# Performance work log

Measured on AMD Instinct MI355X. Metric: run time of the kernel, lower is better.

Reference implementation:

```python
import jax, jax.numpy as jnp
import numpy as np

N_NODES = 100000
N_EDGES = 1600000
IN_FEAT = 128
HID_FEAT = 128
OUT_FEAT = 128


def setup_inputs() -> dict:
    key = jax.random.key(0)
    k1, k2, k3, k4, k5 = jax.random.split(key, 5)
    x = jax.random.normal(k1, (N_NODES, IN_FEAT), dtype=jnp.float32)
    # Xavier-ish scale for weights
    W_in = jax.random.normal(k2, (2, IN_FEAT, HID_FEAT), dtype=jnp.float32) * (1.0 / np.sqrt(IN_FEAT))
    W_out = jax.random.normal(k3, (2, HID_FEAT, OUT_FEAT), dtype=jnp.float32) * (1.0 / np.sqrt(HID_FEAT))
    src = jax.random.randint(k4, (N_EDGES,), 0, N_NODES, dtype=jnp.int32)
    dst = jax.random.randint(k5, (N_EDGES,), 0, N_NODES, dtype=jnp.int32)
    return {"x": x, "W_in": W_in, "W_out": W_out, "src": src, "dst": dst}


def _mean_aggregate(h, src, dst, num_nodes):
    # copy_src('h','m') + fn.mean('m','neigh'): gather src feats, segment-mean by dst.
    msgs = h[src]                                             # [E, D]
    summed = jax.ops.segment_sum(msgs, dst, num_segments=num_nodes)   # [N, D]
    deg = jax.ops.segment_sum(jnp.ones((src.shape[0],), h.dtype), dst,
                              num_segments=num_nodes)         # [N]
    deg = jnp.maximum(deg, 1.0)                               # zero-in-degree -> 0 output
    return summed / deg[:, None]


def reference(x, W_in, W_out, src, dst):
    n = x.shape[0]
    # Layer 0 (i == 0): uses weight_in, ReLU activation (i != K-1)
    neigh = _mean_aggregate(x, src, dst, n)
    h = x @ W_in[0] + neigh @ W_in[1]
    h = jax.nn.relu(h)
    # Layer 1 (i == K-1): uses weight_out, no activation
    neigh = _mean_aggregate(h, src, dst, n)
    h = h @ W_out[0] + neigh @ W_out[1]
    return h
```

## Files before the change

### kernel.cpp

```cpp
#include <hip/hip_runtime.h>

#define NF 128
#define NBSHIFT 8
#define NBMAX 512
#define CHUNK 4096
#define DCHUNK 4096

typedef __attribute__((ext_vector_type(8))) short bf16x8;
typedef __attribute__((ext_vector_type(4))) float f32x4;
typedef __attribute__((ext_vector_type(2))) float f32x2;

__device__ __forceinline__ unsigned short f2bf(float f) {
    unsigned int u = __builtin_bit_cast(unsigned int, f);
    u = (u + 0x7fffu + ((u >> 16) & 1u)) >> 16;
    return (unsigned short)u;
}
__device__ __forceinline__ float bflo(unsigned int u) {
    return __builtin_bit_cast(float, u << 16);
}
__device__ __forceinline__ float bfhi(unsigned int u) {
    return __builtin_bit_cast(float, u & 0xffff0000u);
}
__device__ __forceinline__ unsigned char f2fp8(float v) {
    return (unsigned char)(__builtin_amdgcn_cvt_pk_fp8_f32(v, v, 0, false) & 0xff);
}

__global__ void k_zero(int* __restrict__ a, int na, int* __restrict__ b, int nb) {
    int i = blockIdx.x * blockDim.x + threadIdx.x;
    if (i < na) a[i] = 0;
    if (i < nb) b[i] = 0;
}

#define BH 256
#define BT 256
__global__ __launch_bounds__(256) void k_prep(const int* __restrict__ dst, int E, int NB,
                                              int* __restrict__ gbhist,
                                              const float* __restrict__ x,
                                              unsigned short* __restrict__ xb,
                                              unsigned char* __restrict__ xq,
                                              const float* __restrict__ Win,
                                              const float* __restrict__ Wout,
                                              unsigned short* __restrict__ BtIn,
                                              unsigned short* __restrict__ BtOut) {
    __shared__ int lh[NBMAX];
    const int bb = blockIdx.x;
    const int t = threadIdx.x;
    if (bb < BH) {
        for (int k = t; k < NBMAX; k += 256) lh[k] = 0;
        __syncthreads();
        for (int i = bb * 256 + t; i < E; i += BH * 256)
            atomicAdd(&lh[((unsigned)dst[i]) >> NBSHIFT], 1);
        __syncthreads();
        for (int k = t; k < NB; k += 256)
            if (lh[k]) atomicAdd(&gbhist[k], lh[k]);
    } else if (bb < BH + BT) {
        int b2 = bb - BH;
        const float* W = (b2 < 128) ? Win : Wout;
        unsigned short* Bt = (b2 < 128) ? BtIn : BtOut;
        int idx = (b2 & 127) * 256 + t;
        int c = idx >> 8;
        int k = idx & 255;
        int p = k >> 7, kk = k & 127;
        Bt[idx] = f2bf(W[((size_t)p * NF + kk) * NF + c]);
    } else {
        long long i = (long long)(bb - BH - BT) * 256 + t;
        const float4 a = *reinterpret_cast<const float4*>(x + i * 8);
        const float4 b = *reinterpret_cast<const float4*>(x + i * 8 + 4);
        union { unsigned short s[8]; uint4 u; } o;
        o.s[0] = f2bf(a.x); o.s[1] = f2bf(a.y); o.s[2] = f2bf(a.z); o.s[3] = f2bf(a.w);
        o.s[4] = f2bf(b.x); o.s[5] = f2bf(b.y); o.s[6] = f2bf(b.z); o.s[7] = f2bf(b.w);
        *reinterpret_cast<uint4*>(xb + i * 8) = o.u;
        int lo = __builtin_amdgcn_cvt_pk_fp8_f32(a.x, a.y, 0, false);
        lo = __builtin_amdgcn_cvt_pk_fp8_f32(a.z, a.w, lo, true);
        int hi = __builtin_amdgcn_cvt_pk_fp8_f32(b.x, b.y, 0, false);
        hi = __builtin_amdgcn_cvt_pk_fp8_f32(b.z, b.w, hi, true);
        uint2 oq; oq.x = (unsigned)lo; oq.y = (unsigned)hi;
        *reinterpret_cast<uint2*>(xq + i * 8) = oq;
    }
}


__global__ __launch_bounds__(256) void k_bscan(const int* __restrict__ gbhist,
                                               int* __restrict__ bbase, int* __restrict__ gcursor,
                                               int NB, int E, int* __restrict__ offsets, int n) {
    __shared__ int sA[NBMAX], sB[NBMAX];
    int t = threadIdx.x;
    for (int k = t; k < NBMAX; k += 256) sA[k] = (k < NB) ? gbhist[k] : 0;
    __syncthreads();
    int* pin = sA;
    int* pout = sB;
    for (int off = 1; off < NBMAX; off <<= 1) {
        for (int k = t; k < NBMAX; k += 256) pout[k] = pin[k] + (k >= off ? pin[k - off] : 0);
        __syncthreads();
        int* tmp = pin; pin = pout; pout = tmp;
    }
    for (int k = t; k < NB; k += 256) {
        int excl = pin[k] - gbhist[k];
        bbase[k] = excl;
        gcursor[k] = excl;
    }
    if (t == 0) {
        bbase[NB] = E;
        offsets[n] = E;
    }
}

__global__ __launch_bounds__(256) void k_bucket(const int* __restrict__ src,
                                                const int* __restrict__ dst,
                                                int* __restrict__ gcursor,
                                                unsigned* __restrict__ gpairs, int E) {
    __shared__ int lhist[NBMAX], lbase[NBMAX], lcur[NBMAX], gb[NBMAX];
    __shared__ int sA[NBMAX], sB[NBMAX];
    __shared__ unsigned stage[CHUNK];
    __shared__ unsigned short stage_b[CHUNK];
    const int t = threadIdx.x;
    const int c0 = blockIdx.x * CHUNK;
    const int cc = min(CHUNK, E - c0);

    for (int k = t; k < NBMAX; k += 256) lhist[k] = 0;
    __syncthreads();

    int ls[16], ld[16];
#pragma unroll
    for (int j = 0; j < 16; ++j) {
        int i = t + j * 256;
        ls[j] = 0; ld[j] = 0;
        if (i < cc) {
            ls[j] = src[c0 + i];
            ld[j] = dst[c0 + i];
            atomicAdd(&lhist[((unsigned)ld[j]) >> NBSHIFT], 1);
        }
    }
    __syncthreads();
    for (int k = t; k < NBMAX; k += 256) sA[k] = lhist[k];
    __syncthreads();
    int* pin = sA;
    int* pout = sB;
    for (int off = 1; off < NBMAX; off <<= 1) {
        for (int k = t; k < NBMAX; k += 256) pout[k] = pin[k] + (k >= off ? pin[k - off] : 0);
        __syncthreads();
        int* tmp = pin; pin = pout; pout = tmp;
    }
    for (int k = t; k < NBMAX; k += 256) {
        int excl = pin[k] - lhist[k];
        lbase[k] = excl;
        lcur[k] = excl;
        int cnt = lhist[k];
        if (cnt > 0) gb[k] = atomicAdd(&gcursor[k], cnt);
    }
    __syncthreads();
#pragma unroll
    for (int j = 0; j < 16; ++j) {
        int i = t + j * 256;
        if (i < cc) {
            int b = ((unsigned)ld[j]) >> NBSHIFT;
            int pos = atomicAdd(&lcur[b], 1);
            stage[pos] = (((unsigned)ld[j] & 255u) << 24) | (unsigned)ls[j];
            stage_b[pos] = (unsigned short)b;
        }
    }
    __syncthreads();
    for (int idx = t; idx < cc; idx += 256) {
        unsigned p = stage[idx];
        int b = stage_b[idx];
        gpairs[gb[b] + (idx - lbase[b])] = p;
    }
}

__global__ __launch_bounds__(256) void k_bsort(const unsigned* __restrict__ gpairs,
                                               const int* __restrict__ bbase,
                                               int* __restrict__ offsets,
                                               float* __restrict__ invdeg,
                                               unsigned char* __restrict__ degb,
                                               int* __restrict__ gdhist,
                                               int* __restrict__ esrc, int n) {
    __shared__ int lcnt[256], lcur[256], sA[256], sB[256], ldh[256];
    const int b = blockIdx.x;
    const int t = threadIdx.x;
    const int base = bbase[b];
    const int c = bbase[b + 1] - base;
    const int n0 = b << NBSHIFT;

    lcnt[t] = 0;
    ldh[t] = 0;
    __syncthreads();
    for (int i = t; i < c; i += 256) {
        int node = (int)(gpairs[base + i] >> 24);
        atomicAdd(&lcnt[node], 1);
    }
    __syncthreads();
    sA[t] = lcnt[t];
    __syncthreads();
    int* pin = sA;
    int* pout = sB;
    for (int off = 1; off < 256; off <<= 1) {
        pout[t] = pin[t] + (t >= off ? pin[t - off] : 0);
        __syncthreads();
        int* tmp = pin; pin = pout; pout = tmp;
    }
    int excl = pin[t] - lcnt[t];
    lcur[t] = excl;
    int node_g = n0 + t;
    if (node_g < n) {
        offsets[node_g] = base + excl;
        invdeg[node_g] = 1.0f / (float)max(lcnt[t], 1);
        int d = min(lcnt[t], 255);
        degb[node_g] = (unsigned char)d;
        atomicAdd(&ldh[d], 1);
    }
    __syncthreads();
    if (ldh[t] > 0) atomicAdd(&gdhist[t], ldh[t]);
    for (int i = t; i < c; i += 256) {
        unsigned p = gpairs[base + i];
        int node = (int)(p >> 24);
        int pos = atomicAdd(&lcur[node], 1);
        esrc[base + pos] = (int)(p & 0x00ffffffu);
    }
}

__global__ void k_dscan(const int* __restrict__ gdhist, int* __restrict__ dcur) {
    __shared__ int sh[256];
    int t = threadIdx.x;
    int v = gdhist[t];
    sh[t] = v;
    __syncthreads();
    for (int off = 1; off < 256; off <<= 1) {
        int x = (t >= off) ? sh[t - off] : 0;
        __syncthreads();
        sh[t] += x;
        __syncthreads();
    }
    dcur[t] = sh[t] - v;
}

__global__ __launch_bounds__(256) void k_dorder(const unsigned char* __restrict__ degb,
                                                int* __restrict__ dcur,
                                                int* __restrict__ dorder, int n) {
    __shared__ int lhist[256], lbase[256], lcur[256], gb[256], sA[256], sB[256];
    __shared__ int stageN[DCHUNK];
    __shared__ unsigned char stageD[DCHUNK];
    const int t = threadIdx.x;
    const int c0 = blockIdx.x * DCHUNK;
    const int cc = min(DCHUNK, n - c0);

    lhist[t] = 0;
    __syncthreads();
    int dloc[16];
#pragma unroll
    for (int j = 0; j < 16; ++j) {
        int i = t + j * 256;
        dloc[j] = -1;
        if (i < cc) {
            dloc[j] = degb[c0 + i];
            atomicAdd(&lhist[dloc[j]], 1);
        }
    }
    __syncthreads();
    sA[t] = lhist[t];
    __syncthreads();
    int* pin = sA;
    int* pout = sB;
    for (int off = 1; off < 256; off <<= 1) {
        pout[t] = pin[t] + (t >= off ? pin[t - off] : 0);
        __syncthreads();
        int* tmp = pin; pin = pout; pout = tmp;
    }
    int excl = pin[t] - lhist[t];
    lbase[t] = excl;
    lcur[t] = excl;
    if (lhist[t] > 0) gb[t] = atomicAdd(&dcur[t], lhist[t]);
    __syncthreads();
#pragma unroll
    for (int j = 0; j < 16; ++j) {
        int i = t + j * 256;
        if (i < cc) {
            int d = dloc[j];
            int pos = atomicAdd(&lcur[d], 1);
            stageN[pos] = c0 + i;
            stageD[pos] = (unsigned char)d;
        }
    }
    __syncthreads();
    for (int idx = t; idx < cc; idx += 256) {
        int d = stageD[idx];
        dorder[gb[d] + (idx - lbase[d])] = stageN[idx];
    }
}

__global__ __launch_bounds__(256) void k_agg8(const unsigned char* __restrict__ feat,
                                              const int* __restrict__ esrc,
                                              const int* __restrict__ offsets,
                                              const float* __restrict__ invdeg,
                                              const int* __restrict__ dorder,
                                              unsigned short* __restrict__ neigh, int n) {
    const int tid = threadIdx.x;
    const int wv = (int)(((long long)blockIdx.x * blockDim.x + tid) >> 6);
    if (wv * 8 >= n) return;
    const int lane = tid & 63;
    const int g = lane >> 3;
    const int q = lane & 7;
    const int i8 = wv * 8 + g;

    int node = 0, beg = 0, deg = 0;
    if (i8 < n) {
        node = dorder[i8];
        beg = offsets[node];
        deg = offsets[node + 1] - beg;
    }
    int mn = deg, mx = deg;
    int s;
    s = __shfl_xor(mn, 8);  mn = min(mn, s);
    s = __shfl_xor(mx, 8);  mx = max(mx, s);
    s = __shfl_xor(mn, 16); mn = min(mn, s);
    s = __shfl_xor(mx, 16); mx = max(mx, s);
    s = __shfl_xor(mn, 32); mn = min(mn, s);
    s = __shfl_xor(mx, 32); mx = max(mx, s);
    const int mindeg = __builtin_amdgcn_readfirstlane(mn);
    const int maxdeg = __builtin_amdgcn_readfirstlane(mx);

    const unsigned qoff = (unsigned)q * 16u;
    f32x2 acc[8];
#pragma unroll
    for (int j = 0; j < 8; ++j) acc[j] = (f32x2){0.f, 0.f};

    int i = 0;
    for (; i + 4 <= mindeg; i += 4) {
        int e0 = esrc[beg + i + 0];
        int e1 = esrc[beg + i + 1];
        int e2 = esrc[beg + i + 2];
        int e3 = esrc[beg + i + 3];
        uint4 v0 = *(const uint4*)(feat + (unsigned)e0 * 128u + qoff);
        uint4 v1 = *(const uint4*)(feat + (unsigned)e1 * 128u + qoff);
        uint4 v2 = *(const uint4*)(feat + (unsigned)e2 * 128u + qoff);
        uint4 v3 = *(const uint4*)(feat + (unsigned)e3 * 128u + qoff);
#define ACC8(v)                                                       \
        acc[0] += __builtin_amdgcn_cvt_pk_f32_fp8((int)(v).x, false); \
        acc[1] += __builtin_amdgcn_cvt_pk_f32_fp8((int)(v).x, true);  \
        acc[2] += __builtin_amdgcn_cvt_pk_f32_fp8((int)(v).y, false); \
        acc[3] += __builtin_amdgcn_cvt_pk_f32_fp8((int)(v).y, true);  \
        acc[4] += __builtin_amdgcn_cvt_pk_f32_fp8((int)(v).z, false); \
        acc[5] += __builtin_amdgcn_cvt_pk_f32_fp8((int)(v).z, true);  \
        acc[6] += __builtin_amdgcn_cvt_pk_f32_fp8((int)(v).w, false); \
        acc[7] += __builtin_amdgcn_cvt_pk_f32_fp8((int)(v).w, true);
        ACC8(v0) ACC8(v1) ACC8(v2) ACC8(v3)
    }
    for (; i < maxdeg; ++i) {
        if (i < deg) {
            int e = esrc[beg + i];
            uint4 v = *(const uint4*)(feat + (unsigned)e * 128u + qoff);
            ACC8(v)
        }
    }
#undef ACC8

    if (i8 < n) {
        const float sc = invdeg[node];
        unsigned p[8];
#pragma unroll
        for (int j = 0; j < 8; ++j) {
            float ca = acc[j].x * sc, cb = acc[j].y * sc;
            asm("v_cvt_pk_bf16_f32 %0, %1, %2" : "=v"(p[j]) : "v"(ca), "v"(cb));
        }
        char* outb = (char*)neigh + (size_t)node * 256 + (unsigned)q * 32u;
        uint4 o0; o0.x = p[0]; o0.y = p[1]; o0.z = p[2]; o0.w = p[3];
        uint4 o1; o1.x = p[4]; o1.y = p[5]; o1.z = p[6]; o1.w = p[7];
        *(uint4*)outb = o0;
        *(uint4*)(outb + 16) = o1;
    }
}

__global__ __launch_bounds__(256) void k_agg_bf16(const unsigned short* __restrict__ feat,
                                                  const int* __restrict__ esrc,
                                                  const int* __restrict__ offsets,
                                                  const float* __restrict__ invdeg,
                                                  unsigned short* __restrict__ neigh, int n) {
    int wid0 = (int)(((long long)blockIdx.x * blockDim.x + threadIdx.x) >> 6);
    const int wid = __builtin_amdgcn_readfirstlane(wid0);
    if (wid >= n) return;
    const int lane = threadIdx.x & 63;
    const int g = lane >> 4;
    const int q = lane & 15;
    const unsigned qoff = (unsigned)q * 16u;
    const char* fb = (const char*)feat;
    const int beg = offsets[wid];
    const int end = offsets[wid + 1];
    float a0 = 0.f, a1 = 0.f, a2 = 0.f, a3 = 0.f, a4 = 0.f, a5 = 0.f, a6 = 0.f, a7 = 0.f;
    int i = beg;
    for (; i + 4 <= end; i += 4) {
        int e0 = esrc[i + 0], e1 = esrc[i + 1], e2 = esrc[i + 2], e3 = esrc[i + 3];
        int es = (g & 2) ? ((g & 1) ? e3 : e2) : ((g & 1) ? e1 : e0);
        uint4 v = *(const uint4*)(fb + (unsigned)es * 256u + qoff);
        a0 += bflo(v.x); a1 += bfhi(v.x);
        a2 += bflo(v.y); a3 += bfhi(v.y);
        a4 += bflo(v.z); a5 += bfhi(v.z);
        a6 += bflo(v.w); a7 += bfhi(v.w);
    }
    if (i < end) {
        int r = end - i;
        if (g < r) {
            int es = esrc[i + g];
            uint4 v = *(const uint4*)(fb + (unsigned)es * 256u + qoff);
            a0 += bflo(v.x); a1 += bfhi(v.x);
            a2 += bflo(v.y); a3 += bfhi(v.y);
            a4 += bflo(v.z); a5 += bfhi(v.z);
            a6 += bflo(v.w); a7 += bfhi(v.w);
        }
    }
    a0 += __shfl_xor(a0, 16); a1 += __shfl_xor(a1, 16);
    a2 += __shfl_xor(a2, 16); a3 += __shfl_xor(a3, 16);
    a4 += __shfl_xor(a4, 16); a5 += __shfl_xor(a5, 16);
    a6 += __shfl_xor(a6, 16); a7 += __shfl_xor(a7, 16);
    a0 += __shfl_xor(a0, 32); a1 += __shfl_xor(a1, 32);
    a2 += __shfl_xor(a2, 32); a3 += __shfl_xor(a3, 32);
    a4 += __shfl_xor(a4, 32); a5 += __shfl_xor(a5, 32);
    a6 += __shfl_xor(a6, 32); a7 += __shfl_xor(a7, 32);
    const float sc = invdeg[wid];
    a0 *= sc; a1 *= sc; a2 *= sc; a3 *= sc;
    a4 *= sc; a5 *= sc; a6 *= sc; a7 *= sc;
    unsigned p0, p1, p2, p3;
    asm("v_cvt_pk_bf16_f32 %0, %1, %2" : "=v"(p0) : "v"(a0), "v"(a1));
    asm("v_cvt_pk_bf16_f32 %0, %1, %2" : "=v"(p1) : "v"(a2), "v"(a3));
    asm("v_cvt_pk_bf16_f32 %0, %1, %2" : "=v"(p2) : "v"(a4), "v"(a5));
    asm("v_cvt_pk_bf16_f32 %0, %1, %2" : "=v"(p3) : "v"(a6), "v"(a7));
    if (g == 0) {
        uint4 o; o.x = p0; o.y = p1; o.z = p2; o.w = p3;
        *(uint4*)((char*)neigh + (size_t)wid * 256 + qoff) = o;
    }
}

__global__ __launch_bounds__(256) void k_agg_f32(const float* __restrict__ feat,
                                                 const int* __restrict__ esrc,
                                                 const int* __restrict__ offsets,
                                                 const float* __restrict__ invdeg,
                                                 unsigned short* __restrict__ neigh, int n) {
    int wid0 = (int)(((long long)blockIdx.x * blockDim.x + threadIdx.x) >> 6);
    const int wid = __builtin_amdgcn_readfirstlane(wid0);
    if (wid >= n) return;
    int lane = threadIdx.x & 63;
    int beg = offsets[wid], end = offsets[wid + 1];
    float a0 = 0.f, a1 = 0.f;
    for (int i = beg; i < end; ++i) {
        int s0 = esrc[i];
        float2 v0 = *(const float2*)(feat + (size_t)s0 * NF + lane * 2);
        a0 += v0.x; a1 += v0.y;
    }
    float sc = invdeg[wid];
    unsigned pk;
    float ca = a0 * sc, cb = a1 * sc;
    asm("v_cvt_pk_bf16_f32 %0, %1, %2" : "=v"(pk) : "v"(ca), "v"(cb));
    *(unsigned*)(neigh + (size_t)wid * NF + lane * 2) = pk;
}

template <bool RELU, bool OUTBF16, bool WRITEQ>
__global__ __launch_bounds__(256) void k_gemm_lds(const unsigned short* __restrict__ A1,
                                                  const unsigned short* __restrict__ A2,
                                                  const unsigned short* __restrict__ Bt,
                                                  void* __restrict__ outv,
                                                  unsigned char* __restrict__ outq,
                                                  int nrows) {
    __shared__ __align__(16) unsigned char sm[32768];
    const int tid = threadIdx.x;
    const int w = tid >> 6;
    const int lane = tid & 63;
    const int l15 = lane & 15;
    const int lk = lane >> 4;
    const int col0 = w * 32;
    const int rbase = blockIdx.x * 64;

#pragma unroll
    for (int h = 0; h < 2; ++h) {
        const unsigned short* Ah = h ? A2 : A1;
#pragma unroll
        for (int j = 0; j < 4; ++j) {
            const int r = w * 16 + j * 4 + lk;
            const int garow = min(rbase + r, nrows - 1);
            const int cch = l15 ^ (r & 7);
            const unsigned short* srcp = Ah + (size_t)garow * NF + cch * 8;
            unsigned char* ldst = &sm[h * 16384 + (w * 16 + j * 4) * 256];
            __builtin_amdgcn_global_load_lds(
                (const __attribute__((address_space(1))) void*)srcp,
                (__attribute__((address_space(3))) void*)ldst, 16, 0, 0);
        }
    }

    bf16x8 breg[2][8];
#pragma unroll
    for (int c = 0; c < 2; ++c)
#pragma unroll
        for (int kc = 0; kc < 8; ++kc)
            breg[c][kc] = *(const bf16x8*)(Bt + (size_t)(col0 + c * 16 + l15) * 256 +
                                           kc * 32 + lk * 8);

    f32x4 acc[4][2];
#pragma unroll
    for (int rc = 0; rc < 4; ++rc) {
        acc[rc][0] = (f32x4)0.0f;
        acc[rc][1] = (f32x4)0.0f;
    }

    __syncthreads();

#pragma unroll
    for (int rc = 0; rc < 4; ++rc) {
        const int row = rc * 16 + l15;
#pragma unroll
        for (int kc = 0; kc < 8; ++kc) {
            const int half = kc >> 2;
            const int kk = kc & 3;
            const int chunk = (kk * 4 + lk) ^ (row & 7);
            const bf16x8 a = *(const bf16x8*)&sm[half * 16384 + row * 256 + chunk * 16];
            acc[rc][0] = __builtin_amdgcn_mfma_f32_16x16x32_bf16(a, breg[0][kc],
                                                                 acc[rc][0], 0, 0, 0);
            acc[rc][1] = __builtin_amdgcn_mfma_f32_16x16x32_bf16(a, breg[1][kc],
                                                                 acc[rc][1], 0, 0, 0);
        }
    }

    __syncthreads();

    if (OUTBF16) {
        unsigned short* smb = (unsigned short*)sm;
        unsigned char* smq = sm + 16384;
#pragma unroll
        for (int rc = 0; rc < 4; ++rc)
#pragma unroll
            for (int r = 0; r < 4; ++r) {
                const int row = rc * 16 + lk * 4 + r;
#pragma unroll
                for (int c = 0; c < 2; ++c) {
                    float v = acc[rc][c][r];
                    if (RELU) v = fmaxf(v, 0.f);
                    const int col = col0 + c * 16 + l15;
                    smb[row * NF + col] = f2bf(v);
                    if (WRITEQ) smq[row * NF + col] = f2fp8(v);
                }
            }
        __syncthreads();
#pragma unroll
        for (int it = 0; it < 4; ++it) {
            const int off = (tid + it * 256) * 16;
            if (rbase + (off >> 8) < nrows)
                *(uint4*)((char*)outv + (size_t)rbase * 256 + off) =
                    *(const uint4*)&sm[off];
        }
        if (WRITEQ) {
#pragma unroll
            for (int it = 0; it < 2; ++it) {
                const int off = (tid + it * 256) * 16;
                if (rbase + (off >> 7) < nrows)
                    *(uint4*)(outq + (size_t)rbase * 128 + off) =
                        *(const uint4*)&sm[16384 + off];
            }
        }
    } else {
        float* smf = (float*)sm;
#pragma unroll
        for (int rc = 0; rc < 4; ++rc)
#pragma unroll
            for (int r = 0; r < 4; ++r) {
                const int row = rc * 16 + lk * 4 + r;
#pragma unroll
                for (int c = 0; c < 2; ++c) {
                    float v = acc[rc][c][r];
                    if (RELU) v = fmaxf(v, 0.f);
                    smf[row * NF + col0 + c * 16 + l15] = v;
                }
            }
        __syncthreads();
#pragma unroll
        for (int it = 0; it < 8; ++it) {
            const int off = (tid + it * 256) * 16;
            if (rbase + (off >> 9) < nrows)
                *(uint4*)((char*)outv + (size_t)rbase * 512 + off) =
                    *(const uint4*)&sm[off];
        }
    }
}

template <bool RELU, bool A1BF16, bool OUTBF16>
__global__ __launch_bounds__(256) void k_gemm_mfma(const void* __restrict__ A1v,
                                                   const unsigned short* __restrict__ A2,
                                                   const unsigned short* __restrict__ Bt,
                                                   void* __restrict__ outv, int nrows) {
    const int tid = threadIdx.x;
    const int wave = tid >> 6;
    const int lane = tid & 63;
    const int l15 = lane & 15;
    const int lk = lane >> 4;
    const int col0 = wave * 32;
    const int rbase = blockIdx.x * 64;

    bf16x8 breg[2][8];
#pragma unroll
    for (int c = 0; c < 2; ++c)
#pragma unroll
        for (int kc = 0; kc < 8; ++kc)
            breg[c][kc] = *(const bf16x8*)(Bt + (size_t)(col0 + c * 16 + l15) * 256 +
                                           kc * 32 + lk * 8);

    f32x4 acc[4][2];
#pragma unroll
    for (int rc = 0; rc < 4; ++rc) {
        acc[rc][0] = (f32x4)0.0f;
        acc[rc][1] = (f32x4)0.0f;
    }

#pragma unroll
    for (int rc = 0; rc < 4; ++rc) {
        const int arow = rbase + rc * 16 + l15;
        const bool ok = arow < nrows;
        bf16x8 a[8];
        if (ok) {
            if (A1BF16) {
                const unsigned short* A1 = (const unsigned short*)A1v;
#pragma unroll
                for (int kc = 0; kc < 4; ++kc) {
                    a[kc] = *(const bf16x8*)(A1 + (size_t)arow * NF + kc * 32 + lk * 8);
                    a[kc + 4] = *(const bf16x8*)(A2 + (size_t)arow * NF + kc * 32 + lk * 8);
                }
            } else {
                const float* A1 = (const float*)A1v;
#pragma unroll
                for (int kc = 0; kc < 4; ++kc) {
                    const float* p = A1 + (size_t)arow * NF + kc * 32 + lk * 8;
                    float4 u = *(const float4*)p;
                    float4 v = *(const float4*)(p + 4);
                    a[kc][0] = (short)f2bf(u.x); a[kc][1] = (short)f2bf(u.y);
                    a[kc][2] = (short)f2bf(u.z); a[kc][3] = (short)f2bf(u.w);
                    a[kc][4] = (short)f2bf(v.x); a[kc][5] = (short)f2bf(v.y);
                    a[kc][6] = (short)f2bf(v.z); a[kc][7] = (short)f2bf(v.w);
                    a[kc + 4] = *(const bf16x8*)(A2 + (size_t)arow * NF + kc * 32 + lk * 8);
                }
            }
        } else {
#pragma unroll
            for (int kc = 0; kc < 8; ++kc) a[kc] = (bf16x8)(short)0;
        }
#pragma unroll
        for (int kc = 0; kc < 8; ++kc) {
            acc[rc][0] = __builtin_amdgcn_mfma_f32_16x16x32_bf16(a[kc], breg[0][kc],
                                                                 acc[rc][0], 0, 0, 0);
            acc[rc][1] = __builtin_amdgcn_mfma_f32_16x16x32_bf16(a[kc], breg[1][kc],
                                                                 acc[rc][1], 0, 0, 0);
        }
    }

#pragma unroll
    for (int rc = 0; rc < 4; ++rc) {
#pragma unroll
        for (int r = 0; r < 4; ++r) {
            const int orow = rbase + rc * 16 + lk * 4 + r;
            if (orow >= nrows) continue;
#pragma unroll
            for (int c = 0; c < 2; ++c) {
                float v = acc[rc][c][r];
                if (RELU) v = fmaxf(v, 0.f);
                const int col = col0 + c * 16 + l15;
                if (OUTBF16)
                    ((unsigned short*)outv)[(size_t)orow * NF + col] = f2bf(v);
                else
                    ((float*)outv)[(size_t)orow * NF + col] = v;
            }
        }
    }
}

extern "C" void kernel_launch(void* const* d_in, const int* in_sizes, int n_in,
                              void* d_out, int out_size, void* d_ws, size_t ws_size,
                              hipStream_t stream) {
    const float* x = (const float*)d_in[0];
    const float* W_in = (const float*)d_in[1];
    const float* W_out = (const float*)d_in[2];
    const int* src = (const int*)d_in[3];
    const int* dst = (const int*)d_in[4];

    const int n = in_sizes[0] / NF;
    const int E = in_sizes[3];
    float* outp = (float*)d_out;

    const int NB = (n + 255) >> NBSHIFT;
    const int nchunks = (E + CHUNK - 1) / CHUNK;

    char* ws = (char*)d_ws;
    size_t off = 0;
    auto take = [&](size_t bytes) {
        void* p = ws + off;
        off = (off + bytes + 511) & ~(size_t)511;
        return p;
    };
    int* gbhist = (int*)take((size_t)NB * 4);
    int* bbase = (int*)take((size_t)(NB + 1) * 4);
    int* gcursor = (int*)take((size_t)NB * 4);
    int* offsets = (int*)take((size_t)(n + 1) * 4);
    float* invdeg = (float*)take((size_t)n * 4);
    unsigned short* BtIn = (unsigned short*)take(128 * 256 * 2);
    unsigned short* BtOut = (unsigned short*)take(128 * 256 * 2);
    unsigned* gpairs = (unsigned*)take((size_t)E * 4);
    int* esrc = (int*)take((size_t)E * 4);
    unsigned short* hb = (unsigned short*)take((size_t)n * NF * 2);
    unsigned short* neigh = (unsigned short*)take((size_t)n * NF * 2);
    unsigned char* degb = (unsigned char*)take((size_t)n);
    int* gdhist = (int*)take(256 * 4);
    int* dcur = (int*)take(256 * 4);
    int* dorder = (int*)take((size_t)n * 4);
    size_t need_fp8 = off + (size_t)n * NF * 2 + 512 + (size_t)n * NF + 512 +
                      (size_t)n * NF + 512;
    bool use_fp8 = (ws_size >= need_fp8);
    unsigned short* xb = nullptr;
    unsigned char* xq = nullptr;
    unsigned char* hq = nullptr;
    if (use_fp8) {
        xb = (unsigned short*)take((size_t)n * NF * 2);
        xq = (unsigned char*)take((size_t)n * NF);
        hq = (unsigned char*)take((size_t)n * NF);
    }
    bool use_xb = use_fp8 || (ws_size >= off + (size_t)n * NF * 2);
    if (!use_fp8 && use_xb) xb = (unsigned short*)take((size_t)n * NF * 2);

    k_zero<<<(max(NB, 256) + 255) / 256, 256, 0, stream>>>(gbhist, NB, gdhist, 256);

    const int cvtBlocks = use_fp8 ? (int)(((long long)n * NF / 8 + 255) / 256) : 0;
    k_prep<<<BH + BT + cvtBlocks, 256, 0, stream>>>(dst, E, NB, gbhist, x, xb, xq,
                                                    W_in, W_out, BtIn, BtOut);
    k_bscan<<<1, 256, 0, stream>>>(gbhist, bbase, gcursor, NB, E, offsets, n);
    k_bucket<<<nchunks, 256, 0, stream>>>(src, dst, gcursor, gpairs, E);
    k_bsort<<<NB, 256, 0, stream>>>(gpairs, bbase, offsets, invdeg, degb, gdhist, esrc, n);

    const int gemmBlocks = (n + 63) / 64;

    if (use_fp8) {
        k_dscan<<<1, 256, 0, stream>>>(gdhist, dcur);
        k_dorder<<<(n + DCHUNK - 1) / DCHUNK, 256, 0, stream>>>(degb, dcur, dorder, n);

        const int agg8Blocks = (n + 31) / 32;
        k_agg8<<<agg8Blocks, 256, 0, stream>>>(xq, esrc, offsets, invdeg, dorder, neigh, n);
        k_gemm_lds<true, true, true>
            <<<gemmBlocks, 256, 0, stream>>>(xb, neigh, BtIn, hb, hq, n);
        k_agg8<<<agg8Blocks, 256, 0, stream>>>(hq, esrc, offsets, invdeg, dorder, neigh, n);
        k_gemm_lds<false, false, false>
            <<<gemmBlocks, 256, 0, stream>>>(hb, neigh, BtOut, outp, nullptr, n);
    } else {
        const int aggBlocks = (n + 3) / 4;
        k_agg_f32<<<aggBlocks, 256, 0, stream>>>(x, esrc, offsets, invdeg, neigh, n);
        k_gemm_mfma<true, false, true>
            <<<gemmBlocks, 256, 0, stream>>>(x, neigh, BtIn, hb, n);
        k_agg_bf16<<<aggBlocks, 256, 0, stream>>>(hb, esrc, offsets, invdeg, neigh, n);
        k_gemm_mfma<false, true, false>
            <<<gemmBlocks, 256, 0, stream>>>(hb, neigh, BtOut, outp, n);
    }
}
```

Measured before the change: 196.9 us.

## Sort nodes by degree locally inside bucket sort, drop global degree-order kernels

Replaces the global degree histogram, scan and degree-ordering kernels with a per-bucket (256-node) degree sort done inside k_bsort, writing dorder directly. This removes two kernel launches and a pass over the degree array, at the cost of only a local rather than global degree ordering for load balance in the aggregation kernels. Also enlarges the bucketing chunk from 4096 to 6144 edges per block, which raises per-thread register arrays and shared memory use.

```diff
diff --git a/kernel.cpp b/kernel.cpp
--- a/kernel.cpp
+++ b/kernel.cpp
@@ -3,8 +3,7 @@
 #define NF 128
 #define NBSHIFT 8
 #define NBMAX 512
-#define CHUNK 4096
-#define DCHUNK 4096
+#define CHUNK 6144
 
 typedef __attribute__((ext_vector_type(8))) short bf16x8;
 typedef __attribute__((ext_vector_type(4))) float f32x4;
@@ -25,10 +24,9 @@
     return (unsigned char)(__builtin_amdgcn_cvt_pk_fp8_f32(v, v, 0, false) & 0xff);
 }
 
-__global__ void k_zero(int* __restrict__ a, int na, int* __restrict__ b, int nb) {
+__global__ void k_zero(int* __restrict__ a, int na) {
     int i = blockIdx.x * blockDim.x + threadIdx.x;
     if (i < na) a[i] = 0;
-    if (i < nb) b[i] = 0;
 }
 
 #define BH 256
@@ -120,9 +118,9 @@
     for (int k = t; k < NBMAX; k += 256) lhist[k] = 0;
     __syncthreads();
 
-    int ls[16], ld[16];
-#pragma unroll
-    for (int j = 0; j < 16; ++j) {
+    int ls[24], ld[24];
+#pragma unroll
+    for (int j = 0; j < 24; ++j) {
         int i = t + j * 256;
         ls[j] = 0; ld[j] = 0;
         if (i < cc) {
@@ -150,7 +148,7 @@
     }
     __syncthreads();
 #pragma unroll
-    for (int j = 0; j < 16; ++j) {
+    for (int j = 0; j < 24; ++j) {
         int i = t + j * 256;
         if (i < cc) {
             int b = ((unsigned)ld[j]) >> NBSHIFT;
@@ -171,10 +169,9 @@
                                                const int* __restrict__ bbase,
                                                int* __restrict__ offsets,
                                                float* __restrict__ invdeg,
-                                               unsigned char* __restrict__ degb,
-                                               int* __restrict__ gdhist,
+                                               int* __restrict__ dorder,
                                                int* __restrict__ esrc, int n) {
-    __shared__ int lcnt[256], lcur[256], sA[256], sB[256], ldh[256];
+    __shared__ int lcnt[256], lcur[256], sA[256], sB[256], dh[256], dc[256];
     const int b = blockIdx.x;
     const int t = threadIdx.x;
     const int base = bbase[b];
@@ -182,7 +179,7 @@
     const int n0 = b << NBSHIFT;
 
     lcnt[t] = 0;
-    ldh[t] = 0;
+    dh[t] = 0;
     __syncthreads();
     for (int i = t; i < c; i += 256) {
         int node = (int)(gpairs[base + i] >> 24);
@@ -198,92 +195,38 @@
         __syncthreads();
         int* tmp = pin; pin = pout; pout = tmp;
     }
-    int excl = pin[t] - lcnt[t];
+    const int deg = lcnt[t];
+    const int excl = pin[t] - deg;
     lcur[t] = excl;
-    int node_g = n0 + t;
-    if (node_g < n) {
+    const int node_g = n0 + t;
+    const bool valid = node_g < n;
+    const int dcap = min(deg, 255);
+    if (valid) {
         offsets[node_g] = base + excl;
-        invdeg[node_g] = 1.0f / (float)max(lcnt[t], 1);
-        int d = min(lcnt[t], 255);
-        degb[node_g] = (unsigned char)d;
-        atomicAdd(&ldh[d], 1);
-    }
-    __syncthreads();
-    if (ldh[t] > 0) atomicAdd(&gdhist[t], ldh[t]);
+        invdeg[node_g] = 1.0f / (float)max(deg, 1);
+        atomicAdd(&dh[dcap], 1);
+    }
+    __syncthreads();
+    sA[t] = dh[t];
+    __syncthreads();
+    pin = sA;
+    pout = sB;
+    for (int off = 1; off < 256; off <<= 1) {
+        pout[t] = pin[t] + (t >= off ? pin[t - off] : 0);
+        __syncthreads();
+        int* tmp = pin; pin = pout; pout = tmp;
+    }
+    dc[t] = pin[t] - dh[t];
+    __syncthreads();
+    if (valid) {
+        int pos = atomicAdd(&dc[dcap], 1);
+        dorder[n0 + pos] = node_g;
+    }
     for (int i = t; i < c; i += 256) {
         unsigned p = gpairs[base + i];
         int node = (int)(p >> 24);
         int pos = atomicAdd(&lcur[node], 1);
         esrc[base + pos] = (int)(p & 0x00ffffffu);
-    }
-}
-
-__global__ void k_dscan(const int* __restrict__ gdhist, int* __restrict__ dcur) {
-    __shared__ int sh[256];
-    int t = threadIdx.x;
-    int v = gdhist[t];
-    sh[t] = v;
-    __syncthreads();
-    for (int off = 1; off < 256; off <<= 1) {
-        int x = (t >= off) ? sh[t - off] : 0;
-        __syncthreads();
-        sh[t] += x;
-        __syncthreads();
-    }
-    dcur[t] = sh[t] - v;
-}
-
-__global__ __launch_bounds__(256) void k_dorder(const unsigned char* __restrict__ degb,
-                                                int* __restrict__ dcur,
-                                                int* __restrict__ dorder, int n) {
-    __shared__ int lhist[256], lbase[256], lcur[256], gb[256], sA[256], sB[256];
-    __shared__ int stageN[DCHUNK];
-    __shared__ unsigned char stageD[DCHUNK];
-    const int t = threadIdx.x;
-    const int c0 = blockIdx.x * DCHUNK;
-    const int cc = min(DCHUNK, n - c0);
-
-    lhist[t] = 0;
-    __syncthreads();
-    int dloc[16];
-#pragma unroll
-    for (int j = 0; j < 16; ++j) {
-        int i = t + j * 256;
-        dloc[j] = -1;
-        if (i < cc) {
-            dloc[j] = degb[c0 + i];
-            atomicAdd(&lhist[dloc[j]], 1);
-        }
-    }
-    __syncthreads();
-    sA[t] = lhist[t];
-    __syncthreads();
-    int* pin = sA;
-    int* pout = sB;
-    for (int off = 1; off < 256; off <<= 1) {
-        pout[t] = pin[t] + (t >= off ? pin[t - off] : 0);
-        __syncthreads();
-        int* tmp = pin; pin = pout; pout = tmp;
-    }
-    int excl = pin[t] - lhist[t];
-    lbase[t] = excl;
-    lcur[t] = excl;
-    if (lhist[t] > 0) gb[t] = atomicAdd(&dcur[t], lhist[t]);
-    __syncthreads();
-#pragma unroll
-    for (int j = 0; j < 16; ++j) {
-        int i = t + j * 256;
-        if (i < cc) {
-            int d = dloc[j];
-            int pos = atomicAdd(&lcur[d], 1);
-            stageN[pos] = c0 + i;
-            stageD[pos] = (unsigned char)d;
-        }
-    }
-    __syncthreads();
-    for (int idx = t; idx < cc; idx += 256) {
-        int d = stageD[idx];
-        dorder[gb[d] + (idx - lbase[d])] = stageN[idx];
     }
 }
 
@@ -699,9 +642,6 @@
     int* esrc = (int*)take((size_t)E * 4);
     unsigned short* hb = (unsigned short*)take((size_t)n * NF * 2);
     unsigned short* neigh = (unsigned short*)take((size_t)n * NF * 2);
-    unsigned char* degb = (unsigned char*)take((size_t)n);
-    int* gdhist = (int*)take(256 * 4);
-    int* dcur = (int*)take(256 * 4);
     int* dorder = (int*)take((size_t)n * 4);
     size_t need_fp8 = off + (size_t)n * NF * 2 + 512 + (size_t)n * NF + 512 +
                       (size_t)n * NF + 512;
@@ -717,21 +657,18 @@
     bool use_xb = use_fp8 || (ws_size >= off + (size_t)n * NF * 2);
     if (!use_fp8 && use_xb) xb = (unsigned short*)take((size_t)n * NF * 2);
 
-    k_zero<<<(max(NB, 256) + 255) / 256, 256, 0, stream>>>(gbhist, NB, gdhist, 256);
+    k_zero<<<(NB + 255) / 256, 256, 0, stream>>>(gbhist, NB);
 
     const int cvtBlocks = use_fp8 ? (int)(((long long)n * NF / 8 + 255) / 256) : 0;
     k_prep<<<BH + BT + cvtBlocks, 256, 0, stream>>>(dst, E, NB, gbhist, x, xb, xq,
                                                     W_in, W_out, BtIn, BtOut);
     k_bscan<<<1, 256, 0, stream>>>(gbhist, bbase, gcursor, NB, E, offsets, n);
     k_bucket<<<nchunks, 256, 0, stream>>>(src, dst, gcursor, gpairs, E);
-    k_bsort<<<NB, 256, 0, stream>>>(gpairs, bbase, offsets, invdeg, degb, gdhist, esrc, n);
+    k_bsort<<<NB, 256, 0, stream>>>(gpairs, bbase, offsets, invdeg, dorder, esrc, n);
 
     const int gemmBlocks = (n + 63) / 64;
 
     if (use_fp8) {
-        k_dscan<<<1, 256, 0, stream>>>(gdhist, dcur);
-        k_dorder<<<(n + DCHUNK - 1) / DCHUNK, 256, 0, stream>>>(degb, dcur, dorder, n);
-
         const int agg8Blocks = (n + 31) / 32;
         k_agg8<<<agg8Blocks, 256, 0, stream>>>(xq, esrc, offsets, invdeg, dorder, neigh, n);
         k_gemm_lds<true, true, true>
```

Measured after the change: 201.6 us. 2.4% more time.
